# Performance work log

Measured on AMD Instinct MI355X. Metric: run time of the kernel, lower is better.

## Reference

```python
import jax, jax.numpy as jnp
import numpy as np

B, L, F = 256, 512, 64
NUM_IDS = 2000
LN_EPS = 1e-5


def setup_inputs() -> dict:
    key = jax.random.key(0)
    ks = jax.random.split(key, 16)
    s = 0.05
    return {
        # padded neighbor-id sequences; 0 is the padding id
        "src_ids": jax.random.randint(ks[0], (B, L), 0, NUM_IDS, dtype=jnp.int64)
        if jax.config.jax_enable_x64 else jax.random.randint(ks[0], (B, L), 0, NUM_IDS, dtype=jnp.int32),
        "dst_ids": jax.random.randint(ks[1], (B, L), 0, NUM_IDS, dtype=jnp.int64)
        if jax.config.jax_enable_x64 else jax.random.randint(ks[1], (B, L), 0, NUM_IDS, dtype=jnp.int32),
        # co-occurrence encode MLP: Linear(1->F), ReLU, Linear(F->F)
        "enc_w1": jax.random.normal(ks[2], (1, F), jnp.float32) * s,
        "enc_b1": jax.random.normal(ks[3], (F,), jnp.float32) * s,
        "enc_w2": jax.random.normal(ks[4], (F, F), jnp.float32) * s,
        "enc_b2": jax.random.normal(ks[5], (F,), jnp.float32) * s,
        # cross-attention projections (bias-free q/k/v as in source)
        "Wq": jax.random.normal(ks[6], (F, F), jnp.float32) * s,
        "Wk": jax.random.normal(ks[7], (F, F), jnp.float32) * s,
        "Wv": jax.random.normal(ks[8], (F, F), jnp.float32) * s,
        "Wo": jax.random.normal(ks[9], (F, F), jnp.float32) * s,
        "bo": jax.random.normal(ks[10], (F,), jnp.float32) * s,
        "ln_g": jnp.ones((F,), jnp.float32),
        "ln_b": jnp.zeros((F,), jnp.float32),
    }


def _counts_in(a, b):
    # for each element of a: how many times does it occur in b (same batch row)
    # equivalent to the np.unique count / mapping-dict lookup in the original
    return (a[:, :, None] == b[:, None, :]).sum(axis=-1).astype(jnp.float32)


def _appearances(a, b):
    # [B, L, 2]: counts of each id of `a` in (a, b); zero out padding (id==0)
    app = jnp.stack([_counts_in(a, a), _counts_in(a, b)], axis=-1)
    return jnp.where((a == 0)[..., None], 0.0, app)


def _encode(app, w1, b1, w2, b2):
    # Linear(1->F) -> ReLU -> Linear(F->F), then sum over the 2 count channels
    h = jax.nn.relu(app[..., None] * w1[0] + b1)  # [B, L, 2, F]
    h = jnp.einsum('blcf,fg->blcg', h, w2) + b2
    return h.sum(axis=2)  # [B, L, F]


def _linear_attn(q, k, v):
    dim = q.shape[-1]
    q = jax.nn.softmax(q, axis=-1) * (dim ** -0.5)
    k = jax.nn.softmax(k, axis=1)  # softmax over sequence dim (dim=-2)
    ctx = jnp.einsum('bld,ble->bde', k, v)
    return jnp.einsum('bld,bde->ble', q, ctx)


def _layer_norm(x, g, b):
    mu = x.mean(axis=-1, keepdims=True)
    var = ((x - mu) ** 2).mean(axis=-1, keepdims=True)
    return (x - mu) * jax.lax.rsqrt(var + LN_EPS) * g + b


def _cross_attn(x, ctx, Wq, Wk, Wv, Wo, bo, ln_g, ln_b):
    q, k, v = x @ Wq, ctx @ Wk, ctx @ Wv
    attn = _linear_attn(q, k, v)
    return _layer_norm(x + attn @ Wo + bo, ln_g, ln_b)


def reference(src_ids, dst_ids, enc_w1, enc_b1, enc_w2, enc_b2,
              Wq, Wk, Wv, Wo, bo, ln_g, ln_b):
    # neighbor co-occurrence counting + encoding
    src_app = _appearances(src_ids, dst_ids)  # [B, L, 2]
    dst_app = _appearances(dst_ids, src_ids)
    src_feat = _encode(src_app, enc_w1, enc_b1, enc_w2, enc_b2)  # [B, L, F]
    dst_feat = _encode(dst_app, enc_w1, enc_b1, enc_w2, enc_b2)
    # linear cross-attention fusion (shared weights, both directions)
    src_out = _cross_attn(src_feat, dst_feat, Wq, Wk, Wv, Wo, bo, ln_g, ln_b)
    dst_out = _cross_attn(dst_feat, src_feat, Wq, Wk, Wv, Wo, bo, ln_g, ln_b)
    return jnp.stack([src_out, dst_out])  # [2, B, L, F]
```

## Files before the change

kernel.cpp:

```cpp
#include <hip/hip_runtime.h>

#define BB 256
#define LL 512

typedef float nfloat4 __attribute__((ext_vector_type(4)));
typedef int   nint4   __attribute__((ext_vector_type(4)));

__global__ __launch_bounds__(256, 2) void k_all(
    const int* __restrict__ src, const int* __restrict__ dst,
    const float* __restrict__ w1, const float* __restrict__ b1,
    const float* __restrict__ w2, const float* __restrict__ b2,
    const float* __restrict__ Wq, const float* __restrict__ Wk,
    const float* __restrict__ Wv, const float* __restrict__ Wo,
    const float* __restrict__ bo, const float* __restrict__ lng,
    const float* __restrict__ lnb, float* __restrict__ out) {
  __shared__ __align__(16) char smem[63776];
  int*   hist  = (int*)smem;
  float* poolF = (float*)smem;
  int*   dmapc = (int*)(smem + 16384);
  float* tabL  = (float*)(smem + 16384);
  int*   dmapx = (int*)(smem + 32768);
  float* Mg    = (float*)(smem + 32768);
  int*   xkey  = (int*)(smem + 50176);
  int*   ckey  = (int*)(smem + 52224);
  int*   cmult = (int*)(smem + 54272);
  int*   pidxl = (int*)(smem + 56320);
  int*   cflag = (int*)(smem + 58368);
  int*   clist = (int*)(smem + 60424);
  float* fbF   = (float*)(smem + 60688);
  int*   npp   = (int*)(smem + 63760);

  int bd = blockIdx.x, b = bd >> 1, dir = bd & 1;
  int tid = threadIdx.x, tx = tid & 63, ty = tid >> 6;
  int e0 = ty * 16;

  const int* s = src + b * LL;
  const int* d = dst + b * LL;
  int sid0 = s[tid], sid1 = s[tid + 256];
  int did0 = d[tid], did1 = d[tid + 256];

  float wcA[64], wcB[64];
#pragma unroll
  for (int f = 0; f < 64; ++f) wcA[f] = w2[f * 64 + tx];
  float w1v = w1[tx], b1v = b1[tx], b2v = b2[tx];

  {
    nint4 z4 = {0, 0, 0, 0};
    nint4* h4z = (nint4*)hist;
    for (int i = tid; i < 500; i += 256) h4z[i] = z4;
    nint4* dm4 = (nint4*)dmapc;
    for (int i = tid; i < 2048; i += 256) dm4[i] = z4;
    nint4* cf4 = (nint4*)cflag;
    if (tid < 128) cf4[tid] = z4;
    if (tid == 0) cflag[512] = 0;
    if (tid < 3) npp[tid] = 0;
  }
  __syncthreads();

  atomicAdd(&hist[sid0], 1);      atomicAdd(&hist[sid1], 1);
  atomicAdd(&hist[did0], 65536);  atomicAdd(&hist[did1], 65536);
  __syncthreads();

  int x0 = dir ? did0 : sid0, x1 = dir ? did1 : sid1;

  for (int i = tid; i < 2000; i += 256) {
    int hv = hist[i];
    if (i != 0 && hv != 0) { cflag[hv & 0xffff] = 1; cflag[hv >> 16] = 1; }
  }
  if (tid == 0) cflag[0] = 1;
  __syncthreads();

  for (int c = tid; c < 513; c += 256) {
    if (cflag[c]) {
      int idx = atomicAdd(&npp[2], 1);
      clist[idx] = c;
      cflag[c] = idx;
    }
  }
  __syncthreads();

  for (int i = tid; i < 2000; i += 256) {
    int hv = hist[i];
    if (i == 0 || hv == 0) continue;
    int cs = hv & 0xffff, cd = hv >> 16;
    int k = cflag[min(cs, cd)] * 64 + cflag[max(cs, cd)];
    int ox = dir ? cd : cs;
    int oc = dir ? cs : cd;
    if (ox) dmapx[k] = 1;
    if (oc) atomicAdd(&dmapc[k], oc);
  }
  if (tid == 0) {
    int hv = hist[0];
    int cs = hv & 0xffff, cd = hv >> 16;
    int k00 = cflag[0] * 65;
    int ox = dir ? cd : cs, oc = dir ? cs : cd;
    if (ox) dmapx[k00] = 1;
    if (oc) atomicAdd(&dmapc[k00], oc);
  }
  __syncthreads();

  for (int i = tid; i < 4096; i += 256) {
    int v = dmapc[i];
    if (v) { int idx = atomicAdd(&npp[0], 1); ckey[idx] = i; cmult[idx] = v; }
    int xv = dmapx[i];
    if (xv) { int idx = atomicAdd(&npp[1], 1); xkey[idx] = i; dmapx[i] = idx; }
  }
  __syncthreads();
  int Pc = npp[0], Px = npp[1], nc = npp[2];

  {
    int hvx0 = (x0 == 0) ? 0 : hist[x0];
    int hvx1 = (x1 == 0) ? 0 : hist[x1];
    int k0, k1;
    {
      int cs = hvx0 & 0xffff, cd = hvx0 >> 16;
      k0 = (x0 == 0) ? cflag[0] * 65 : cflag[min(cs, cd)] * 64 + cflag[max(cs, cd)];
    }
    {
      int cs = hvx1 & 0xffff, cd = hvx1 >> 16;
      k1 = (x1 == 0) ? cflag[0] * 65 : cflag[min(cs, cd)] * 64 + cflag[max(cs, cd)];
    }
    pidxl[tid]       = dmapx[k0];
    pidxl[tid + 256] = dmapx[k1];
  }
  for (int i = ty; i < nc; i += 4) {
    float c = (float)clist[i];
    fbF[ty * 64 + tx] = fmaxf(c * w1v + b1v, 0.f);
    float acc = b2v;
    const float4* h4 = (const float4*)&fbF[ty * 64];
#pragma unroll
    for (int q = 0; q < 16; ++q) {
      float4 hv = h4[q];
      acc += hv.x * wcA[4 * q] + hv.y * wcA[4 * q + 1] + hv.z * wcA[4 * q + 2] + hv.w * wcA[4 * q + 3];
    }
    tabL[i * 64 + tx] = acc;
  }
#pragma unroll
  for (int f = 0; f < 64; ++f) { wcA[f] = Wk[f * 64 + tx]; wcB[f] = Wv[f * 64 + tx]; }
  float macc[16];
#pragma unroll
  for (int e = 0; e < 16; ++e) macc[e] = 0.f;
  float sacc = 0.f;
  __syncthreads();

  float* pA = poolF;
  float* vA = poolF + 2048;
  for (int j0 = 0; j0 < Pc; j0 += 32) {
    int cN = min(32, Pc - j0);
    for (int j = ty; j < cN; j += 4) {
      int key = ckey[j0 + j];
      int ia = key >> 6, ib = key & 63;
      fbF[ty * 64 + tx] = tabL[ia * 64 + tx] + tabL[ib * 64 + tx];
      float kr = 0.f, vr = 0.f;
      const float4* fb4 = (const float4*)&fbF[ty * 64];
#pragma unroll
      for (int q = 0; q < 16; ++q) {
        float4 fv = fb4[q];
        kr += fv.x * wcA[4 * q] + fv.y * wcA[4 * q + 1] + fv.z * wcA[4 * q + 2] + fv.w * wcA[4 * q + 3];
        vr += fv.x * wcB[4 * q] + fv.y * wcB[4 * q + 1] + fv.z * wcB[4 * q + 2] + fv.w * wcB[4 * q + 3];
      }
      float p = __expf(kr) * (float)cmult[j0 + j];
      sacc += p;
      pA[j * 64 + tx] = p;
      vA[j * 64 + tx] = vr;
    }
    if (j0 + 32 >= Pc) fbF[512 + ty * 64 + tx] = sacc;
    __syncthreads();
    for (int jj = 0; jj < cN; ++jj) {
      float pg = pA[jj * 64 + tx];
      const float4* vb4 = (const float4*)&vA[jj * 64 + e0];
#pragma unroll
      for (int q = 0; q < 4; ++q) {
        float4 vv = vb4[q];
        macc[4 * q]     += pg * vv.x; macc[4 * q + 1] += pg * vv.y;
        macc[4 * q + 2] += pg * vv.z; macc[4 * q + 3] += pg * vv.w;
      }
    }
    __syncthreads();
  }
  float inv = 1.f / (fbF[512 + tx] + fbF[576 + tx] + fbF[640 + tx] + fbF[704 + tx]);
#pragma unroll
  for (int e = 0; e < 16; ++e) Mg[(e0 + e) * 68 + tx] = macc[e] * inv;
#pragma unroll
  for (int f = 0; f < 64; ++f) { wcA[f] = Wq[f * 64 + tx]; wcB[f] = Wo[f * 64 + tx]; }
  float bov = bo[tx], lg = lng[tx], lb = lnb[tx];
  __syncthreads();

  for (int i0 = 0; i0 < Px; i0 += 64) {
    int cN = min(64, Px - i0);
    for (int jj = ty; jj < cN; jj += 4) {
      int key = xkey[i0 + jj];
      int ia = key >> 6, ib = key & 63;
      float fv = tabL[ia * 64 + tx] + tabL[ib * 64 + tx];
      fbF[ty * 64 + tx] = fv;
      float qr = 0.f;
      const float4* fb4 = (const float4*)&fbF[ty * 64];
#pragma unroll
      for (int q = 0; q < 16; ++q) {
        float4 f4v = fb4[q];
        qr += f4v.x * wcA[4 * q] + f4v.y * wcA[4 * q + 1] + f4v.z * wcA[4 * q + 2] + f4v.w * wcA[4 * q + 3];
      }
      float p = __expf(qr);
      float sum = p;
#pragma unroll
      for (int off = 32; off >= 1; off >>= 1) sum += __shfl_xor(sum, off, 64);
      float qh = p / sum * 0.125f;
      fbF[256 + ty * 64 + tx] = qh;
      float t = 0.f;
      const float4* qb4 = (const float4*)&fbF[256 + ty * 64];
      const float4* mt4 = (const float4*)&Mg[tx * 68];
#pragma unroll
      for (int q = 0; q < 16; ++q) {
        float4 qv = qb4[q];
        float4 mv = mt4[q];
        t += qv.x * mv.x + qv.y * mv.y + qv.z * mv.z + qv.w * mv.w;
      }
      fbF[512 + ty * 64 + tx] = t;
      float at = 0.f;
      const float4* tb4 = (const float4*)&fbF[512 + ty * 64];
#pragma unroll
      for (int q = 0; q < 16; ++q) {
        float4 tv = tb4[q];
        at += tv.x * wcB[4 * q] + tv.y * wcB[4 * q + 1] + tv.z * wcB[4 * q + 2] + tv.w * wcB[4 * q + 3];
      }
      float r = fv + at + bov;
      float mu = r;
#pragma unroll
      for (int off = 32; off >= 1; off >>= 1) mu += __shfl_xor(mu, off, 64);
      mu *= (1.f / 64.f);
      float dv = r - mu;
      float var = dv * dv;
#pragma unroll
      for (int off = 32; off >= 1; off >>= 1) var += __shfl_xor(var, off, 64);
      var *= (1.f / 64.f);
      poolF[jj * 64 + tx] = dv * rsqrtf(var + 1e-5f) * lg + lb;
    }
    __syncthreads();
    const nfloat4* w4 = (const nfloat4*)poolF;
    nfloat4* out4 = (nfloat4*)(out + (size_t)(dir * BB + b) * (LL * 64));
    for (int idx = tid; idx < 512 * 16; idx += 256) {
      int l = idx >> 4, q = idx & 15;
      int pid = pidxl[l];
      if (pid >= i0 && pid < i0 + cN)
        __builtin_nontemporal_store(w4[(pid - i0) * 16 + q], &out4[l * 16 + q]);
    }
    __syncthreads();
  }
}

extern "C" void kernel_launch(void* const* d_in, const int* in_sizes, int n_in,
                              void* d_out, int out_size, void* d_ws, size_t ws_size,
                              hipStream_t stream) {
  const int* src  = (const int*)d_in[0];
  const int* dst  = (const int*)d_in[1];
  const float* w1 = (const float*)d_in[2];
  const float* b1 = (const float*)d_in[3];
  const float* w2 = (const float*)d_in[4];
  const float* b2 = (const float*)d_in[5];
  const float* Wq = (const float*)d_in[6];
  const float* Wk = (const float*)d_in[7];
  const float* Wv = (const float*)d_in[8];
  const float* Wo = (const float*)d_in[9];
  const float* bo = (const float*)d_in[10];
  const float* lng = (const float*)d_in[11];
  const float* lnb = (const float*)d_in[12];
  float* out = (float*)d_out;

  k_all<<<dim3(512), dim3(256), 0, stream>>>(src, dst, w1, b1, w2, b2,
                                             Wq, Wk, Wv, Wo, bo, lng, lnb, out);
}
```

Before: 118.7 us.

## Process both attention directions in one 512-thread block per batch row

Each batch row now gets a single 512-thread block that handles both directions, instead of two 256-thread blocks that each rebuild the histogram, co-occurrence maps and encoder table for one direction. The block builds source and destination dedup maps together, packs both output indices into one word, then loops over the two directions with smaller tiles split across 8 waves. This removes the duplicated preprocessing, but it halves the grid, runs the two directions one after the other, and the launch bounds of 512 threads with 2 blocks per CU may squeeze register budget for the 128 per-thread weight registers, risking spills.

After: 182.8 us. 1.54x slower.

```diff
diff --git a/kernel.cpp b/kernel.cpp
--- a/kernel.cpp
+++ b/kernel.cpp
@@ -6,7 +6,7 @@
 typedef float nfloat4 __attribute__((ext_vector_type(4)));
 typedef int   nint4   __attribute__((ext_vector_type(4)));
 
-__global__ __launch_bounds__(256, 2) void k_all(
+__global__ __launch_bounds__(512, 2) void k_all(
     const int* __restrict__ src, const int* __restrict__ dst,
     const float* __restrict__ w1, const float* __restrict__ b1,
     const float* __restrict__ w2, const float* __restrict__ b2,
@@ -14,237 +14,237 @@
     const float* __restrict__ Wv, const float* __restrict__ Wo,
     const float* __restrict__ bo, const float* __restrict__ lng,
     const float* __restrict__ lnb, float* __restrict__ out) {
-  __shared__ __align__(16) char smem[63776];
-  int*   hist  = (int*)smem;
-  float* poolF = (float*)smem;
-  int*   dmapc = (int*)(smem + 16384);
-  float* tabL  = (float*)(smem + 16384);
-  int*   dmapx = (int*)(smem + 32768);
-  float* Mg    = (float*)(smem + 32768);
-  int*   xkey  = (int*)(smem + 50176);
-  int*   ckey  = (int*)(smem + 52224);
-  int*   cmult = (int*)(smem + 54272);
-  int*   pidxl = (int*)(smem + 56320);
-  int*   cflag = (int*)(smem + 58368);
-  int*   clist = (int*)(smem + 60424);
-  float* fbF   = (float*)(smem + 60688);
-  int*   npp   = (int*)(smem + 63760);
-
-  int bd = blockIdx.x, b = bd >> 1, dir = bd & 1;
+  __shared__ __align__(16) char smem[62752];
+  int*   dmapS = (int*)smem;
+  float* tabL  = (float*)smem;
+  int*   dmapD = (int*)(smem + 16384);
+  float* Mg    = (float*)(smem + 16384);
+  int*   histp = (int*)(smem + 33792);
+  float* poolF = (float*)(smem + 33792);
+  int*   keyS  = (int*)(smem + 46080);
+  int*   multS = (int*)(smem + 48128);
+  int*   keyD  = (int*)(smem + 50176);
+  int*   multD = (int*)(smem + 52224);
+  int*   pidxl = (int*)(smem + 54272);
+  float* fbF   = (float*)(smem + 56320);
+  int*   cflag = (int*)(smem + 60416);
+  int*   clist = (int*)(smem + 62468);
+  int*   npp   = (int*)(smem + 62724);
+
+  int b = blockIdx.x;
   int tid = threadIdx.x, tx = tid & 63, ty = tid >> 6;
-  int e0 = ty * 16;
 
   const int* s = src + b * LL;
   const int* d = dst + b * LL;
-  int sid0 = s[tid], sid1 = s[tid + 256];
-  int did0 = d[tid], did1 = d[tid + 256];
+  int sid = s[tid], did = d[tid];
 
   float wcA[64], wcB[64];
 #pragma unroll
   for (int f = 0; f < 64; ++f) wcA[f] = w2[f * 64 + tx];
   float w1v = w1[tx], b1v = b1[tx], b2v = b2[tx];
+  float bov = bo[tx], lg = lng[tx], lb = lnb[tx];
 
   {
     nint4 z4 = {0, 0, 0, 0};
-    nint4* h4z = (nint4*)hist;
-    for (int i = tid; i < 500; i += 256) h4z[i] = z4;
-    nint4* dm4 = (nint4*)dmapc;
-    for (int i = tid; i < 2048; i += 256) dm4[i] = z4;
-    nint4* cf4 = (nint4*)cflag;
-    if (tid < 128) cf4[tid] = z4;
+    nint4* dm4 = (nint4*)smem;
+    for (int i = tid; i < 2048; i += 512) dm4[i] = z4;
+    nint4* h4z = (nint4*)histp;
+    if (tid < 500) h4z[tid] = z4;
+    if (tid < 128) ((nint4*)cflag)[tid] = z4;
     if (tid == 0) cflag[512] = 0;
-    if (tid < 3) npp[tid] = 0;
-  }
-  __syncthreads();
-
-  atomicAdd(&hist[sid0], 1);      atomicAdd(&hist[sid1], 1);
-  atomicAdd(&hist[did0], 65536);  atomicAdd(&hist[did1], 65536);
-  __syncthreads();
-
-  int x0 = dir ? did0 : sid0, x1 = dir ? did1 : sid1;
-
-  for (int i = tid; i < 2000; i += 256) {
-    int hv = hist[i];
+    if (tid < 4) npp[tid] = 0;
+  }
+  __syncthreads();
+
+  atomicAdd(&histp[sid], 1);
+  atomicAdd(&histp[did], 65536);
+  __syncthreads();
+
+  for (int i = tid; i < 2000; i += 512) {
+    int hv = histp[i];
     if (i != 0 && hv != 0) { cflag[hv & 0xffff] = 1; cflag[hv >> 16] = 1; }
   }
   if (tid == 0) cflag[0] = 1;
   __syncthreads();
 
-  for (int c = tid; c < 513; c += 256) {
-    if (cflag[c]) {
-      int idx = atomicAdd(&npp[2], 1);
-      clist[idx] = c;
-      cflag[c] = idx;
-    }
-  }
-  __syncthreads();
-
-  for (int i = tid; i < 2000; i += 256) {
-    int hv = hist[i];
+  for (int c = tid; c < 513; c += 512) {
+    if (cflag[c]) { int idx = atomicAdd(&npp[2], 1); clist[idx] = c; cflag[c] = idx; }
+  }
+  __syncthreads();
+
+  for (int i = tid; i < 2000; i += 512) {
+    int hv = histp[i];
     if (i == 0 || hv == 0) continue;
     int cs = hv & 0xffff, cd = hv >> 16;
     int k = cflag[min(cs, cd)] * 64 + cflag[max(cs, cd)];
-    int ox = dir ? cd : cs;
-    int oc = dir ? cs : cd;
-    if (ox) dmapx[k] = 1;
-    if (oc) atomicAdd(&dmapc[k], oc);
+    if (cs) atomicAdd(&dmapS[k], cs);
+    if (cd) atomicAdd(&dmapD[k], cd);
   }
   if (tid == 0) {
-    int hv = hist[0];
+    int hv = histp[0];
     int cs = hv & 0xffff, cd = hv >> 16;
     int k00 = cflag[0] * 65;
-    int ox = dir ? cd : cs, oc = dir ? cs : cd;
-    if (ox) dmapx[k00] = 1;
-    if (oc) atomicAdd(&dmapc[k00], oc);
-  }
-  __syncthreads();
-
-  for (int i = tid; i < 4096; i += 256) {
-    int v = dmapc[i];
-    if (v) { int idx = atomicAdd(&npp[0], 1); ckey[idx] = i; cmult[idx] = v; }
-    int xv = dmapx[i];
-    if (xv) { int idx = atomicAdd(&npp[1], 1); xkey[idx] = i; dmapx[i] = idx; }
-  }
-  __syncthreads();
-  int Pc = npp[0], Px = npp[1], nc = npp[2];
+    if (cs) atomicAdd(&dmapS[k00], cs);
+    if (cd) atomicAdd(&dmapD[k00], cd);
+  }
+  __syncthreads();
+
+  for (int i = tid; i < 4096; i += 512) {
+    int vS = dmapS[i];
+    if (vS) { int ix = atomicAdd(&npp[0], 1); keyS[ix] = i; multS[ix] = vS; dmapS[i] = ix; }
+    int vD = dmapD[i];
+    if (vD) { int ix = atomicAdd(&npp[1], 1); keyD[ix] = i; multD[ix] = vD; dmapD[i] = ix; }
+  }
+  __syncthreads();
+  int nS = npp[0], nD = npp[1], nc = npp[2];
 
   {
-    int hvx0 = (x0 == 0) ? 0 : hist[x0];
-    int hvx1 = (x1 == 0) ? 0 : hist[x1];
     int k0, k1;
-    {
-      int cs = hvx0 & 0xffff, cd = hvx0 >> 16;
-      k0 = (x0 == 0) ? cflag[0] * 65 : cflag[min(cs, cd)] * 64 + cflag[max(cs, cd)];
-    }
-    {
-      int cs = hvx1 & 0xffff, cd = hvx1 >> 16;
-      k1 = (x1 == 0) ? cflag[0] * 65 : cflag[min(cs, cd)] * 64 + cflag[max(cs, cd)];
-    }
-    pidxl[tid]       = dmapx[k0];
-    pidxl[tid + 256] = dmapx[k1];
-  }
-  for (int i = ty; i < nc; i += 4) {
+    if (sid == 0) k0 = cflag[0] * 65;
+    else { int hv = histp[sid]; int cs = hv & 0xffff, cd = hv >> 16;
+           k0 = cflag[min(cs, cd)] * 64 + cflag[max(cs, cd)]; }
+    if (did == 0) k1 = cflag[0] * 65;
+    else { int hv = histp[did]; int cs = hv & 0xffff, cd = hv >> 16;
+           k1 = cflag[min(cs, cd)] * 64 + cflag[max(cs, cd)]; }
+    pidxl[tid] = (dmapS[k0] & 0xffff) | (dmapD[k1] << 16);
+  }
+  __syncthreads();
+
+  for (int i = ty; i < nc; i += 8) {
     float c = (float)clist[i];
     fbF[ty * 64 + tx] = fmaxf(c * w1v + b1v, 0.f);
     float acc = b2v;
-    const float4* h4 = (const float4*)&fbF[ty * 64];
+    const float4* h4p = (const float4*)&fbF[ty * 64];
 #pragma unroll
     for (int q = 0; q < 16; ++q) {
-      float4 hv = h4[q];
-      acc += hv.x * wcA[4 * q] + hv.y * wcA[4 * q + 1] + hv.z * wcA[4 * q + 2] + hv.w * wcA[4 * q + 3];
+      float4 hv = h4p[q];
+      acc += hv.x * wcA[4*q] + hv.y * wcA[4*q+1] + hv.z * wcA[4*q+2] + hv.w * wcA[4*q+3];
     }
     tabL[i * 64 + tx] = acc;
   }
 #pragma unroll
   for (int f = 0; f < 64; ++f) { wcA[f] = Wk[f * 64 + tx]; wcB[f] = Wv[f * 64 + tx]; }
-  float macc[16];
-#pragma unroll
-  for (int e = 0; e < 16; ++e) macc[e] = 0.f;
-  float sacc = 0.f;
-  __syncthreads();
-
-  float* pA = poolF;
-  float* vA = poolF + 2048;
-  for (int j0 = 0; j0 < Pc; j0 += 32) {
-    int cN = min(32, Pc - j0);
-    for (int j = ty; j < cN; j += 4) {
-      int key = ckey[j0 + j];
-      int ia = key >> 6, ib = key & 63;
-      fbF[ty * 64 + tx] = tabL[ia * 64 + tx] + tabL[ib * 64 + tx];
-      float kr = 0.f, vr = 0.f;
-      const float4* fb4 = (const float4*)&fbF[ty * 64];
-#pragma unroll
-      for (int q = 0; q < 16; ++q) {
-        float4 fv = fb4[q];
-        kr += fv.x * wcA[4 * q] + fv.y * wcA[4 * q + 1] + fv.z * wcA[4 * q + 2] + fv.w * wcA[4 * q + 3];
-        vr += fv.x * wcB[4 * q] + fv.y * wcB[4 * q + 1] + fv.z * wcB[4 * q + 2] + fv.w * wcB[4 * q + 3];
-      }
-      float p = __expf(kr) * (float)cmult[j0 + j];
-      sacc += p;
-      pA[j * 64 + tx] = p;
-      vA[j * 64 + tx] = vr;
-    }
-    if (j0 + 32 >= Pc) fbF[512 + ty * 64 + tx] = sacc;
+  __syncthreads();
+
+  for (int dir = 0; dir < 2; ++dir) {
+    const int* aKey = dir ? keyS : keyD;
+    const int* aMul = dir ? multS : multD;
+    int Pa = dir ? nS : nD;
+    float macc[8];
+#pragma unroll
+    for (int e = 0; e < 8; ++e) macc[e] = 0.f;
+    float sacc = 0.f;
+    float* pA = poolF;
+    float* vA = poolF + 1536;
+    for (int j0 = 0; j0 < Pa; j0 += 24) {
+      int cN = min(24, Pa - j0);
+      for (int j = ty; j < cN; j += 8) {
+        int key = aKey[j0 + j];
+        int ia = key >> 6, ib = key & 63;
+        fbF[ty * 64 + tx] = tabL[ia * 64 + tx] + tabL[ib * 64 + tx];
+        float kr = 0.f, vr = 0.f;
+        const float4* fb4 = (const float4*)&fbF[ty * 64];
+#pragma unroll
+        for (int q = 0; q < 16; ++q) {
+          float4 fv = fb4[q];
+          kr += fv.x * wcA[4*q] + fv.y * wcA[4*q+1] + fv.z * wcA[4*q+2] + fv.w * wcA[4*q+3];
+          vr += fv.x * wcB[4*q] + fv.y * wcB[4*q+1] + fv.z * wcB[4*q+2] + fv.w * wcB[4*q+3];
+        }
+        float p = __expf(kr) * (float)aMul[j0 + j];
+        sacc += p;
+        pA[j * 64 + tx] = p;
+        vA[j * 64 + tx] = vr;
+      }
+      if (j0 + 24 >= Pa) fbF[512 + ty * 64 + tx] = sacc;
+      __syncthreads();
+      for (int jj = 0; jj < cN; ++jj) {
+        float pg = pA[jj * 64 + tx];
+        const float4* vb4 = (const float4*)&vA[jj * 64 + ty * 8];
+        float4 v0 = vb4[0], v1 = vb4[1];
+        macc[0] += pg * v0.x; macc[1] += pg * v0.y;
+        macc[2] += pg * v0.z; macc[3] += pg * v0.w;
+        macc[4] += pg * v1.x; macc[5] += pg * v1.y;
+        macc[6] += pg * v1.z; macc[7] += pg * v1.w;
+      }
+      __syncthreads();
+    }
+    float csum = 0.f;
+#pragma unroll
+    for (int w = 0; w < 8; ++w) csum += fbF[512 + w * 64 + tx];
+    float inv = 1.f / csum;
+#pragma unroll
+    for (int e = 0; e < 8; ++e) Mg[(ty * 8 + e) * 68 + tx] = macc[e] * inv;
+#pragma unroll
+    for (int f = 0; f < 64; ++f) { wcA[f] = Wq[f * 64 + tx]; wcB[f] = Wo[f * 64 + tx]; }
     __syncthreads();
-    for (int jj = 0; jj < cN; ++jj) {
-      float pg = pA[jj * 64 + tx];
-      const float4* vb4 = (const float4*)&vA[jj * 64 + e0];
-#pragma unroll
-      for (int q = 0; q < 4; ++q) {
-        float4 vv = vb4[q];
-        macc[4 * q]     += pg * vv.x; macc[4 * q + 1] += pg * vv.y;
-        macc[4 * q + 2] += pg * vv.z; macc[4 * q + 3] += pg * vv.w;
-      }
-    }
-    __syncthreads();
-  }
-  float inv = 1.f / (fbF[512 + tx] + fbF[576 + tx] + fbF[640 + tx] + fbF[704 + tx]);
-#pragma unroll
-  for (int e = 0; e < 16; ++e) Mg[(e0 + e) * 68 + tx] = macc[e] * inv;
-#pragma unroll
-  for (int f = 0; f < 64; ++f) { wcA[f] = Wq[f * 64 + tx]; wcB[f] = Wo[f * 64 + tx]; }
-  float bov = bo[tx], lg = lng[tx], lb = lnb[tx];
-  __syncthreads();
-
-  for (int i0 = 0; i0 < Px; i0 += 64) {
-    int cN = min(64, Px - i0);
-    for (int jj = ty; jj < cN; jj += 4) {
-      int key = xkey[i0 + jj];
-      int ia = key >> 6, ib = key & 63;
-      float fv = tabL[ia * 64 + tx] + tabL[ib * 64 + tx];
-      fbF[ty * 64 + tx] = fv;
-      float qr = 0.f;
-      const float4* fb4 = (const float4*)&fbF[ty * 64];
-#pragma unroll
-      for (int q = 0; q < 16; ++q) {
-        float4 f4v = fb4[q];
-        qr += f4v.x * wcA[4 * q] + f4v.y * wcA[4 * q + 1] + f4v.z * wcA[4 * q + 2] + f4v.w * wcA[4 * q + 3];
-      }
-      float p = __expf(qr);
-      float sum = p;
-#pragma unroll
-      for (int off = 32; off >= 1; off >>= 1) sum += __shfl_xor(sum, off, 64);
-      float qh = p / sum * 0.125f;
-      fbF[256 + ty * 64 + tx] = qh;
-      float t = 0.f;
-      const float4* qb4 = (const float4*)&fbF[256 + ty * 64];
-      const float4* mt4 = (const float4*)&Mg[tx * 68];
-#pragma unroll
-      for (int q = 0; q < 16; ++q) {
-        float4 qv = qb4[q];
-        float4 mv = mt4[q];
-        t += qv.x * mv.x + qv.y * mv.y + qv.z * mv.z + qv.w * mv.w;
-      }
-      fbF[512 + ty * 64 + tx] = t;
-      float at = 0.f;
-      const float4* tb4 = (const float4*)&fbF[512 + ty * 64];
-#pragma unroll
-      for (int q = 0; q < 16; ++q) {
-        float4 tv = tb4[q];
-        at += tv.x * wcB[4 * q] + tv.y * wcB[4 * q + 1] + tv.z * wcB[4 * q + 2] + tv.w * wcB[4 * q + 3];
-      }
-      float r = fv + at + bov;
-      float mu = r;
-#pragma unroll
-      for (int off = 32; off >= 1; off >>= 1) mu += __shfl_xor(mu, off, 64);
-      mu *= (1.f / 64.f);
-      float dv = r - mu;
-      float var = dv * dv;
-#pragma unroll
-      for (int off = 32; off >= 1; off >>= 1) var += __shfl_xor(var, off, 64);
-      var *= (1.f / 64.f);
-      poolF[jj * 64 + tx] = dv * rsqrtf(var + 1e-5f) * lg + lb;
-    }
-    __syncthreads();
-    const nfloat4* w4 = (const nfloat4*)poolF;
-    nfloat4* out4 = (nfloat4*)(out + (size_t)(dir * BB + b) * (LL * 64));
-    for (int idx = tid; idx < 512 * 16; idx += 256) {
-      int l = idx >> 4, q = idx & 15;
-      int pid = pidxl[l];
-      if (pid >= i0 && pid < i0 + cN)
-        __builtin_nontemporal_store(w4[(pid - i0) * 16 + q], &out4[l * 16 + q]);
-    }
-    __syncthreads();
+
+    const int* bKey = dir ? keyD : keyS;
+    int Pb = dir ? nD : nS;
+    for (int i0 = 0; i0 < Pb; i0 += 32) {
+      int cN = min(32, Pb - i0);
+      for (int jj = ty; jj < cN; jj += 8) {
+        int key = bKey[i0 + jj];
+        int ia = key >> 6, ib = key & 63;
+        float fv = tabL[ia * 64 + tx] + tabL[ib * 64 + tx];
+        fbF[ty * 64 + tx] = fv;
+        float qr = 0.f;
+        const float4* fb4 = (const float4*)&fbF[ty * 64];
+#pragma unroll
+        for (int q = 0; q < 16; ++q) {
+          float4 f4v = fb4[q];
+          qr += f4v.x * wcA[4*q] + f4v.y * wcA[4*q+1] + f4v.z * wcA[4*q+2] + f4v.w * wcA[4*q+3];
+        }
+        float p = __expf(qr);
+        float sum = p;
+#pragma unroll
+        for (int off = 32; off >= 1; off >>= 1) sum += __shfl_xor(sum, off, 64);
+        float qh = p / sum * 0.125f;
+        fbF[512 + ty * 64 + tx] = qh;
+        float t = 0.f;
+        const float4* qb4 = (const float4*)&fbF[512 + ty * 64];
+        const float4* mt4 = (const float4*)&Mg[tx * 68];
+#pragma unroll
+        for (int q = 0; q < 16; ++q) {
+          float4 qv = qb4[q];
+          float4 mv = mt4[q];
+          t += qv.x * mv.x + qv.y * mv.y + qv.z * mv.z + qv.w * mv.w;
+        }
+        fbF[ty * 64 + tx] = t;
+        float at = 0.f;
+        const float4* tb4 = (const float4*)&fbF[ty * 64];
+#pragma unroll
+        for (int q = 0; q < 16; ++q) {
+          float4 tv = tb4[q];
+          at += tv.x * wcB[4*q] + tv.y * wcB[4*q+1] + tv.z * wcB[4*q+2] + tv.w * wcB[4*q+3];
+        }
+        float r = fv + at + bov;
+        float mu = r;
+#pragma unroll
+        for (int off = 32; off >= 1; off >>= 1) mu += __shfl_xor(mu, off, 64);
+        mu *= (1.f / 64.f);
+        float dv = r - mu;
+        float var = dv * dv;
+#pragma unroll
+        for (int off = 32; off >= 1; off >>= 1) var += __shfl_xor(var, off, 64);
+        var *= (1.f / 64.f);
+        poolF[jj * 64 + tx] = dv * rsqrtf(var + 1e-5f) * lg + lb;
+      }
+      __syncthreads();
+      const nfloat4* w4 = (const nfloat4*)poolF;
+      nfloat4* out4 = (nfloat4*)(out + (size_t)(dir * BB + b) * (LL * 64));
+      for (int idx = tid; idx < 512 * 16; idx += 512) {
+        int l = idx >> 4, q = idx & 15;
+        int pw = pidxl[l];
+        int pid = dir ? (pw >> 16) : (pw & 0xffff);
+        if (pid >= i0 && pid < i0 + cN)
+          __builtin_nontemporal_store(w4[(pid - i0) * 16 + q], &out4[l * 16 + q]);
+      }
+      __syncthreads();
+    }
+    if (dir == 0) {
+#pragma unroll
+      for (int f = 0; f < 64; ++f) { wcA[f] = Wk[f * 64 + tx]; wcB[f] = Wv[f * 64 + tx]; }
+    }
   }
 }
 
@@ -266,6 +266,6 @@
   const float* lnb = (const float*)d_in[12];
   float* out = (float*)d_out;
 
-  k_all<<<dim3(512), dim3(256), 0, stream>>>(src, dst, w1, b1, w2, b2,
-                                             Wq, Wk, Wv, Wo, bo, lng, lnb, out);
+  k_all<<<dim3(BB), dim3(512), 0, stream>>>(src, dst, w1, b1, w2, b2,
+                                            Wq, Wk, Wv, Wo, bo, lng, lnb, out);
 }
```
